# Performance work log

Hardware: AMD Instinct MI355X
Metric: run time of the kernel (lower is better)

## Reference

```python
import jax, jax.numpy as jnp
import numpy as np

D_MODEL = 1024
D_K = 1024
D_V = 1024
N_HEAD = 16
EPS = 1e-5
BS, N_TOK = 2, 2048


def setup_inputs() -> dict:
    key = jax.random.key(0)
    ks = jax.random.split(key, 12)
    s = 0.02
    q = jax.random.normal(ks[0], (BS, N_TOK, D_MODEL), jnp.float32)
    k = jax.random.normal(ks[1], (BS, N_TOK, D_MODEL), jnp.float32)
    v = jax.random.normal(ks[2], (BS, N_TOK, D_MODEL), jnp.float32)
    return {
        "q": q, "k": k, "v": v,
        "gamma": jnp.ones((D_MODEL,), jnp.float32),
        "beta": jnp.zeros((D_MODEL,), jnp.float32),
        "Wq": jax.random.normal(ks[3], (D_MODEL, D_K), jnp.float32) * s,
        "bq": jnp.zeros((D_K,), jnp.float32),
        "Wk": jax.random.normal(ks[4], (D_MODEL, D_K), jnp.float32) * s,
        "bk": jnp.zeros((D_K,), jnp.float32),
        "Wv": jax.random.normal(ks[5], (D_MODEL, D_V), jnp.float32) * s,
        "bv": jnp.zeros((D_V,), jnp.float32),
        "Wo": jax.random.normal(ks[6], (D_V, D_MODEL), jnp.float32) * s,
        "bo": jnp.zeros((D_MODEL,), jnp.float32),
    }


def reference(q, k, v, gamma, beta, Wq, bq, Wk, bk, Wv, bv, Wo, bo):
    # NOTE: original module ignores k, v args; self-attention over q.
    bs, n_tok, d_m = q.shape
    d_h = D_K // N_HEAD
    temper = float(np.sqrt(d_h))

    # LayerNorm1d over d_model
    mu = jnp.mean(q, axis=-1, keepdims=True)
    var = jnp.var(q, axis=-1, keepdims=True)
    h = (q - mu) / jnp.sqrt(var + EPS) * gamma + beta

    # projections; head split = chunk along feature dim -> [bs, H, T, d_h]
    qh = (h @ Wq + bq).reshape(bs, n_tok, N_HEAD, d_h).transpose(0, 2, 1, 3)
    kh = (h @ Wk + bk).reshape(bs, n_tok, N_HEAD, d_h).transpose(0, 2, 1, 3)
    vh = jax.nn.relu(h @ Wv + bv).reshape(bs, n_tok, N_HEAD, d_h).transpose(0, 2, 1, 3)

    scores = jnp.einsum('bhqd,bhkd->bhqk', qh, kh) / temper
    # dropout before softmax in train mode; identity in eval (deterministic ref)
    attn = jax.nn.softmax(scores, axis=-1)
    o = jnp.einsum('bhqk,bhkd->bhqd', attn, vh)  # [bs, H, T, d_h]

    # faithful to torch: view(bs, n_tok, -1) with NO head transpose (head-major merge)
    merged = o.reshape(bs, n_tok, N_HEAD * d_h)
    out = merged @ Wo + bo + q  # proj + residual
    return out
```

## Files before the change

kernel.cpp:

```cpp
#include <hip/hip_runtime.h>

typedef __bf16 bf16;
typedef __bf16 bf16x8 __attribute__((ext_vector_type(8)));
typedef __bf16 bf16x4 __attribute__((ext_vector_type(4)));
typedef float  f32x4  __attribute__((ext_vector_type(4)));
typedef float  f32x16 __attribute__((ext_vector_type(16)));
typedef unsigned int u32;
typedef u32 u32x4 __attribute__((ext_vector_type(4)));

#define AS1U(p) ((const __attribute__((address_space(1))) unsigned int*)(p))
#define AS3U(p) ((__attribute__((address_space(3))) unsigned int*)(p))

static __device__ __forceinline__ u32 pack2(float a, float b) {
    unsigned short ua = __builtin_bit_cast(unsigned short, (bf16)a);
    unsigned short ub = __builtin_bit_cast(unsigned short, (bf16)b);
    return (u32)ua | ((u32)ub << 16);
}

__global__ void transpose_cast4_kernel(const float* __restrict__ W0, const float* __restrict__ W1,
                                       const float* __restrict__ W2, const float* __restrict__ W3,
                                       bf16* __restrict__ D0, bf16* __restrict__ D1,
                                       bf16* __restrict__ D2, bf16* __restrict__ D3) {
    __shared__ float tile[32][33];
    const float* W; bf16* D;
    switch (blockIdx.z) {
        case 0: W = W0; D = D0; break;
        case 1: W = W1; D = D1; break;
        case 2: W = W2; D = D2; break;
        default: W = W3; D = D3; break;
    }
    const int bj = blockIdx.x, bi = blockIdx.y;
    const int tx = threadIdx.x, ty = threadIdx.y;
#pragma unroll
    for (int i = 0; i < 4; i++) {
        tile[ty + i * 8][tx] = W[(size_t)(bi * 32 + ty + i * 8) * 1024 + bj * 32 + tx];
    }
    __syncthreads();
#pragma unroll
    for (int i = 0; i < 4; i++) {
        D[(size_t)(bj * 32 + ty + i * 8) * 1024 + bi * 32 + tx] =
            (bf16)tile[tx][ty + i * 8];
    }
}

__global__ void layernorm_kernel(const float* __restrict__ x,
                                 const float* __restrict__ gamma,
                                 const float* __restrict__ beta,
                                 bf16* __restrict__ h) {
    const int row = blockIdx.x;
    const float* xr = x + (size_t)row * 1024;
    const int t = threadIdx.x;
    float4 v = ((const float4*)xr)[t];
    float s  = v.x + v.y + v.z + v.w;
    float s2 = v.x * v.x + v.y * v.y + v.z * v.z + v.w * v.w;
#pragma unroll
    for (int m = 1; m < 64; m <<= 1) {
        s  += __shfl_xor(s, m, 64);
        s2 += __shfl_xor(s2, m, 64);
    }
    __shared__ float ssum[4], ssum2[4];
    const int wid = t >> 6, lane = t & 63;
    if (lane == 0) { ssum[wid] = s; ssum2[wid] = s2; }
    __syncthreads();
    s  = ssum[0] + ssum[1] + ssum[2] + ssum[3];
    s2 = ssum2[0] + ssum2[1] + ssum2[2] + ssum2[3];
    const float mu  = s * (1.f / 1024.f);
    const float var = s2 * (1.f / 1024.f) - mu * mu;
    const float rs  = rsqrtf(var + 1e-5f);
    float4 g = ((const float4*)gamma)[t];
    float4 b = ((const float4*)beta)[t];
    bf16x4 o;
    o[0] = (bf16)((v.x - mu) * rs * g.x + b.x);
    o[1] = (bf16)((v.y - mu) * rs * g.y + b.y);
    o[2] = (bf16)((v.z - mu) * rs * g.z + b.z);
    o[3] = (bf16)((v.w - mu) * rs * g.w + b.w);
    ((bf16x4*)(h + (size_t)row * 1024))[t] = o;
}

template <int EPI>
__global__ void gemm_kernel(const bf16* __restrict__ A, const bf16* __restrict__ BT,
                            int N, int K,
                            bf16* __restrict__ Cb,
                            const float* __restrict__ b0, const float* __restrict__ b1,
                            const float* __restrict__ b2, bf16* __restrict__ Vt,
                            float* __restrict__ Cf, const float* __restrict__ bo,
                            const float* __restrict__ resid) {
    __shared__ bf16 Asm[128][32];
    __shared__ bf16 Bsm[128][32];
    const int tid = threadIdx.x;
    const int lane = tid & 63, wave = tid >> 6;
    const int wr = wave >> 1, wc = wave & 1;
    const int tileN = blockIdx.x * 128, tileM = blockIdx.y * 128;
    const int row16 = lane & 15, g = lane >> 4;

    f32x4 acc[4][4] = {};

    for (int kt = 0; kt < K; kt += 32) {
#pragma unroll
        for (int i = 0; i < 2; i++) {
            int c = tid + i * 256;
            int r = c >> 2, cb = (c & 3) * 16;
            const char* g_ = (const char*)(A + (size_t)(tileM + r) * K + kt) + cb;
            char* l_ = (char*)&Asm[0][0] + c * 16;
            __builtin_amdgcn_global_load_lds(AS1U(g_), AS3U(l_), 16, 0, 0);
        }
#pragma unroll
        for (int i = 0; i < 2; i++) {
            int c = tid + i * 256;
            int r = c >> 2, cb = (c & 3) * 16;
            const char* g_ = (const char*)(BT + (size_t)(tileN + r) * K + kt) + cb;
            char* l_ = (char*)&Bsm[0][0] + c * 16;
            __builtin_amdgcn_global_load_lds(AS1U(g_), AS3U(l_), 16, 0, 0);
        }
        __syncthreads();
        bf16x8 af[4], bfr[4];
#pragma unroll
        for (int m = 0; m < 4; m++)
            af[m] = *(const bf16x8*)&Asm[wr * 64 + m * 16 + row16][g * 8];
#pragma unroll
        for (int n = 0; n < 4; n++)
            bfr[n] = *(const bf16x8*)&Bsm[wc * 64 + n * 16 + row16][g * 8];
#pragma unroll
        for (int m = 0; m < 4; m++)
#pragma unroll
            for (int n = 0; n < 4; n++)
                acc[m][n] = __builtin_amdgcn_mfma_f32_16x16x32_bf16(af[m], bfr[n],
                                                                   acc[m][n], 0, 0, 0);
        __syncthreads();
    }
#pragma unroll
    for (int m = 0; m < 4; m++) {
        const int row = tileM + wr * 64 + m * 16 + g * 4;
#pragma unroll
        for (int n = 0; n < 4; n++) {
            const int col = tileN + wc * 64 + n * 16 + row16;
            if (EPI == 0 && col >= 2048) {
                const int d = col - 2048;
                const float bias = b2[d];
                bf16x4 pk;
#pragma unroll
                for (int j = 0; j < 4; j++) {
                    float v = acc[m][n][j] + bias;
                    pk[j] = (bf16)fmaxf(v, 0.f);
                }
                const int bb = row >> 11, tt = row & 2047;
                const int hh = d >> 6, dd = d & 63;
                *(bf16x4*)&Vt[(((size_t)bb * 16 + hh) * 64 + dd) * 2048 + tt] = pk;
            } else {
#pragma unroll
                for (int j = 0; j < 4; j++) {
                    float v = acc[m][n][j];
                    const int r = row + j;
                    if (EPI == 0) {
                        if (col < 1024) {
                            v = (v + b0[col]) * 0.18033688011112042f;
                        } else {
                            v += b1[col - 1024];
                        }
                        Cb[(size_t)r * N + col] = (bf16)v;
                    } else {
                        v += bo[col] + resid[(size_t)r * N + col];
                        Cf[(size_t)r * N + col] = v;
                    }
                }
            }
        }
    }
}

__global__ __launch_bounds__(512, 4)
void attn_kernel(const bf16* __restrict__ qkv, const bf16* __restrict__ Vt,
                 bf16* __restrict__ Obuf) {
    const int bid = blockIdx.x;
    const int swz = (bid & 7) * 64 + (bid >> 3);
    const int bh = swz >> 4, qt = swz & 15;
    const int b = bh >> 4, h = bh & 15;
    const int qbase = qt * 128;
    const int tid = threadIdx.x;
    const int lane = tid & 63, wv = tid >> 6;
    const int half = wv >> 2, qw = wv & 3;
    const int c = lane & 31, p = lane >> 5;

    __shared__ bf16 Kl[2][2][64][64];
    __shared__ bf16 Vl[2][2][64][64];

    const bf16* qrow = qkv + (size_t)(b * 2048 + qbase + qw * 32 + c) * 3072 + h * 64;
    bf16x8 qf[4];
#pragma unroll
    for (int ch = 0; ch < 4; ch++)
        qf[ch] = *(const bf16x8*)(qrow + ch * 16 + p * 8);

    const char* kgbase = (const char*)(qkv + (size_t)b * 2048 * 3072 + 1024 + h * 64)
                         + (size_t)(half * 1024) * 6144;
    const char* vgbase = (const char*)(Vt + (size_t)bh * 64 * 2048) + half * 2048;
    const int ht = tid & 255;
    const char* kgp[2]; const char* vgp[2]; int ldo[2];
#pragma unroll
    for (int i = 0; i < 2; i++) {
        const int cc = ht + i * 256;
        const int srow = cc >> 3;
        const int scol = ((cc & 7) * 16) ^ ((srow & 7) << 4);
        kgp[i] = kgbase + (size_t)srow * 6144 + scol;
        vgp[i] = vgbase + (size_t)srow * 4096 + scol;
        ldo[i] = cc * 16;
    }
    char* kldb = (char*)&Kl[half][0][0][0];
    char* vldb = (char*)&Vl[half][0][0][0];

    auto stage = [&](int t, int slot) {
        const size_t ko = (size_t)t * (64 * 6144);
        const size_t vo = (size_t)t * 128;
        const int sb = slot * 8192;
#pragma unroll
        for (int i = 0; i < 2; i++) {
            __builtin_amdgcn_global_load_lds(AS1U(kgp[i] + ko), AS3U(kldb + sb + ldo[i]), 16, 0, 0);
            __builtin_amdgcn_global_load_lds(AS1U(vgp[i] + vo), AS3U(vldb + sb + ldo[i]), 16, 0, 0);
        }
    };

    f32x16 accO[2] = {};
    float l_r = 0.f;

    auto compute = [&](int slot) {
        const char* Kb = (const char*)&Kl[half][slot][0][0];
        const char* Vb = (const char*)&Vl[half][slot][0][0];
#pragma unroll
        for (int cc = 0; cc < 2; cc++) {
            f32x16 accT = {};
            const int tok = cc * 32 + c;
#pragma unroll
            for (int ch = 0; ch < 4; ch++) {
                const bf16x8 kf = *(const bf16x8*)(Kb + tok * 128 +
                                                   ((ch * 32 + p * 16) ^ ((tok & 7) << 4)));
                accT = __builtin_amdgcn_mfma_f32_32x32x16_bf16(kf, qf[ch], accT, 0, 0, 0);
            }
            float pv[16];
#pragma unroll
            for (int r = 0; r < 16; r++) pv[r] = exp2f(accT[r]);
            float s01 = (pv[0] + pv[1]) + (pv[2] + pv[3]);
            float s23 = (pv[4] + pv[5]) + (pv[6] + pv[7]);
            float s45 = (pv[8] + pv[9]) + (pv[10] + pv[11]);
            float s67 = (pv[12] + pv[13]) + (pv[14] + pv[15]);
            l_r += (s01 + s23) + (s45 + s67);
            u32 k01 = pack2(pv[0], pv[1]),  k23 = pack2(pv[2], pv[3]);
            u32 k45 = pack2(pv[4], pv[5]),  k67 = pack2(pv[6], pv[7]);
            u32 k89 = pack2(pv[8], pv[9]),  kab = pack2(pv[10], pv[11]);
            u32 kcd = pack2(pv[12], pv[13]), kef = pack2(pv[14], pv[15]);
            asm("v_permlane32_swap_b32 %0, %1" : "+v"(k45), "+v"(k01));
            asm("v_permlane32_swap_b32 %0, %1" : "+v"(k67), "+v"(k23));
            asm("v_permlane32_swap_b32 %0, %1" : "+v"(kcd), "+v"(k89));
            asm("v_permlane32_swap_b32 %0, %1" : "+v"(kef), "+v"(kab));
            u32x4 w0w = {k01, k23, k45, k67};
            u32x4 w1w = {k89, kab, kcd, kef};
            const bf16x8 pf0 = __builtin_bit_cast(bf16x8, w0w);
            const bf16x8 pf1 = __builtin_bit_cast(bf16x8, w1w);
#pragma unroll
            for (int dc = 0; dc < 2; dc++) {
                const int rd = dc * 32 + c;
                const int sw = (rd & 7) << 4;
                const bf16x8 vf0 = *(const bf16x8*)(Vb + rd * 128 + ((cc * 64 + p * 16) ^ sw));
                const bf16x8 vf1 = *(const bf16x8*)(Vb + rd * 128 + ((cc * 64 + 32 + p * 16) ^ sw));
                accO[dc] = __builtin_amdgcn_mfma_f32_32x32x16_bf16(pf0, vf0, accO[dc], 0, 0, 0);
                accO[dc] = __builtin_amdgcn_mfma_f32_32x32x16_bf16(pf1, vf1, accO[dc], 0, 0, 0);
            }
        }
    };

#define KV_SYNC() do { \
        asm volatile("s_waitcnt vmcnt(0)" ::: "memory"); \
        __builtin_amdgcn_s_barrier(); \
        asm volatile("" ::: "memory"); \
    } while (0)

    stage(0, 0);
#pragma unroll 1
    for (int t = 0; t < 14; t += 2) {
        KV_SYNC(); stage(t + 1, 1); compute(0);
        KV_SYNC(); stage(t + 2, 0); compute(1);
    }
    KV_SYNC(); stage(15, 1); compute(0);
    KV_SYNC(); compute(1);
#undef KV_SYNC

    __syncthreads();
    float* ex = (float*)&Kl[0][0][0][0];
    const int xb = (qw * 64 + lane) * 33;
    if (half) {
#pragma unroll
        for (int dc = 0; dc < 2; dc++)
#pragma unroll
            for (int r = 0; r < 16; r++) ex[xb + dc * 16 + r] = accO[dc][r];
        ex[xb + 32] = l_r;
    }
    __syncthreads();
    if (!half) {
#pragma unroll
        for (int dc = 0; dc < 2; dc++)
#pragma unroll
            for (int r = 0; r < 16; r++) accO[dc][r] += ex[xb + dc * 16 + r];
        l_r += ex[xb + 32];
        l_r += __shfl_xor(l_r, 32);
        const float linv = 1.f / l_r;
        float li[16];
#pragma unroll
        for (int r = 0; r < 16; r++)
            li[r] = __shfl(linv, (r & 3) + 8 * (r >> 2) + 4 * p);
        bf16* ob = Obuf + ((size_t)bh * 2048 + qbase + qw * 32) * 64;
#pragma unroll
        for (int dc = 0; dc < 2; dc++)
#pragma unroll
            for (int r = 0; r < 16; r++) {
                const int row = (r & 3) + 8 * (r >> 2) + 4 * p;
                ob[(size_t)row * 64 + dc * 32 + c] = (bf16)(accO[dc][r] * li[r]);
            }
    }
}

extern "C" void kernel_launch(void* const* d_in, const int* in_sizes, int n_in,
                              void* d_out, int out_size, void* d_ws, size_t ws_size,
                              hipStream_t stream) {
    const float* q     = (const float*)d_in[0];
    const float* gamma = (const float*)d_in[3];
    const float* beta  = (const float*)d_in[4];
    const float* Wq    = (const float*)d_in[5];
    const float* bq    = (const float*)d_in[6];
    const float* Wk    = (const float*)d_in[7];
    const float* bk    = (const float*)d_in[8];
    const float* Wv    = (const float*)d_in[9];
    const float* bv    = (const float*)d_in[10];
    const float* Wo    = (const float*)d_in[11];
    const float* bo    = (const float*)d_in[12];
    float* out = (float*)d_out;

    char* ws = (char*)d_ws;
    bf16* h     = (bf16*)(ws);
    bf16* WcatT = (bf16*)(ws + (8u << 20));
    bf16* WoT   = (bf16*)(ws + (14u << 20));
    bf16* qkv   = (bf16*)(ws + (16u << 20));
    bf16* Obuf  = (bf16*)(ws + (40u << 20));
    bf16* Vtb   = (bf16*)(ws + (48u << 20));

    transpose_cast4_kernel<<<dim3(32, 32, 4), dim3(32, 8), 0, stream>>>(
        Wq, Wk, Wv, Wo,
        WcatT, WcatT + (size_t)1024 * 1024, WcatT + (size_t)2048 * 1024, WoT);

    layernorm_kernel<<<4096, 256, 0, stream>>>(q, gamma, beta, h);

    gemm_kernel<0><<<dim3(24, 32), 256, 0, stream>>>(h, WcatT, 3072, 1024,
                                                     qkv, bq, bk, bv, Vtb,
                                                     nullptr, nullptr, nullptr);

    attn_kernel<<<512, 512, 0, stream>>>(qkv, Vtb, Obuf);

    gemm_kernel<1><<<dim3(8, 32), 256, 0, stream>>>(Obuf, WoT, 1024, 1024,
                                                    nullptr, nullptr, nullptr, nullptr, nullptr,
                                                    out, bo, q);
}
```

Measured before the change: 143.5 us.

## Stage QKV GEMM epilogue through swizzled LDS for coalesced stores; remap block order

The QKV projection epilogue now writes biased, scaled and activated results into a per-wave XOR-swizzled LDS tile, then reads them back as 16-byte rows and stores them coalesced to the Q/K buffer or the transposed V buffer. This replaces the old scattered 2-byte and 8-byte strided global stores. The block index is also remapped so that consecutive workgroups are spread in strides of eight across the tile grid, which changes L2 reuse and XCD placement. The cost is an extra 32 KB of shared memory per block, which can lower occupancy, plus an LDS round trip in the epilogue.

New measurement: 131.2 us. 1.09x faster.

```diff
diff --git a/kernel.cpp b/kernel.cpp
--- a/kernel.cpp
+++ b/kernel.cpp
@@ -90,7 +90,11 @@
     const int tid = threadIdx.x;
     const int lane = tid & 63, wave = tid >> 6;
     const int wr = wave >> 1, wc = wave & 1;
-    const int tileN = blockIdx.x * 128, tileM = blockIdx.y * 128;
+    const int nwg = gridDim.x * gridDim.y;
+    const int bid0 = blockIdx.y * gridDim.x + blockIdx.x;
+    const int bid = (bid0 & 7) * (nwg >> 3) + (bid0 >> 3);
+    const int tileN = (bid % gridDim.x) * 128;
+    const int tileM = (bid / gridDim.x) * 128;
     const int row16 = lane & 15, g = lane >> 4;
 
     f32x4 acc[4][4] = {};
@@ -128,40 +132,79 @@
                                                                    acc[m][n], 0, 0, 0);
         __syncthreads();
     }
-#pragma unroll
-    for (int m = 0; m < 4; m++) {
-        const int row = tileM + wr * 64 + m * 16 + g * 4;
-#pragma unroll
-        for (int n = 0; n < 4; n++) {
-            const int col = tileN + wc * 64 + n * 16 + row16;
-            if (EPI == 0 && col >= 2048) {
-                const int d = col - 2048;
-                const float bias = b2[d];
-                bf16x4 pk;
+
+    if constexpr (EPI == 0) {
+        __shared__ bf16 Ep[4][64][64];
+        char* ep = (char*)&Ep[wave][0][0];
+        const bool isV = (tileN >= 2048);
+        if (!isV) {
+#pragma unroll
+            for (int n = 0; n < 4; n++) {
+                const int cl = n * 16 + row16;
+                const int gc = tileN + wc * 64 + cl;
+                const float bias = gc < 1024 ? b0[gc] : b1[gc - 1024];
+                const float scl = gc < 1024 ? 0.18033688011112042f : 1.f;
+#pragma unroll
+                for (int m = 0; m < 4; m++)
+#pragma unroll
+                    for (int j = 0; j < 4; j++) {
+                        const int rl = m * 16 + g * 4 + j;
+                        const float v = (acc[m][n][j] + bias) * scl;
+                        *(bf16*)(ep + rl * 128 + ((cl * 2) ^ ((rl & 7) << 4))) = (bf16)v;
+                    }
+            }
+        } else {
+#pragma unroll
+            for (int n = 0; n < 4; n++) {
+                const int dl = n * 16 + row16;
+                const float bias = b2[(tileN - 2048) + wc * 64 + dl];
+#pragma unroll
+                for (int m = 0; m < 4; m++)
+#pragma unroll
+                    for (int j = 0; j < 4; j++) {
+                        const int tl = m * 16 + g * 4 + j;
+                        const float v = fmaxf(acc[m][n][j] + bias, 0.f);
+                        *(bf16*)(ep + dl * 128 + ((tl * 2) ^ ((dl & 7) << 4))) = (bf16)v;
+                    }
+            }
+        }
+        asm volatile("s_waitcnt lgkmcnt(0)" ::: "memory");
+        __builtin_amdgcn_sched_barrier(0);
+        if (!isV) {
+#pragma unroll
+            for (int it = 0; it < 8; it++) {
+                const int rl = (lane >> 3) + it * 8;
+                const bf16x8 vrow = *(const bf16x8*)(ep + rl * 128 +
+                                                     (((lane & 7) * 16) ^ ((rl & 7) << 4)));
+                const int gr = tileM + wr * 64 + rl;
+                const int gc = tileN + wc * 64 + (lane & 7) * 8;
+                *(bf16x8*)&Cb[(size_t)gr * N + gc] = vrow;
+            }
+        } else {
+            const int bb = tileM >> 11;
+            const int tbase = (tileM & 2047) + wr * 64 + (lane & 7) * 8;
+#pragma unroll
+            for (int it = 0; it < 8; it++) {
+                const int dl = (lane >> 3) + it * 8;
+                const bf16x8 vrow = *(const bf16x8*)(ep + dl * 128 +
+                                                     (((lane & 7) * 16) ^ ((dl & 7) << 4)));
+                const int gd = (tileN - 2048) + wc * 64 + dl;
+                const int hh = gd >> 6, dd = gd & 63;
+                *(bf16x8*)&Vt[(((size_t)bb * 16 + hh) * 64 + dd) * 2048 + tbase] = vrow;
+            }
+        }
+    } else {
+#pragma unroll
+        for (int m = 0; m < 4; m++) {
+            const int row = tileM + wr * 64 + m * 16 + g * 4;
+#pragma unroll
+            for (int n = 0; n < 4; n++) {
+                const int col = tileN + wc * 64 + n * 16 + row16;
 #pragma unroll
                 for (int j = 0; j < 4; j++) {
-                    float v = acc[m][n][j] + bias;
-                    pk[j] = (bf16)fmaxf(v, 0.f);
-                }
-                const int bb = row >> 11, tt = row & 2047;
-                const int hh = d >> 6, dd = d & 63;
-                *(bf16x4*)&Vt[(((size_t)bb * 16 + hh) * 64 + dd) * 2048 + tt] = pk;
-            } else {
-#pragma unroll
-                for (int j = 0; j < 4; j++) {
-                    float v = acc[m][n][j];
                     const int r = row + j;
-                    if (EPI == 0) {
-                        if (col < 1024) {
-                            v = (v + b0[col]) * 0.18033688011112042f;
-                        } else {
-                            v += b1[col - 1024];
-                        }
-                        Cb[(size_t)r * N + col] = (bf16)v;
-                    } else {
-                        v += bo[col] + resid[(size_t)r * N + col];
-                        Cf[(size_t)r * N + col] = v;
-                    }
+                    Cf[(size_t)r * N + col] = acc[m][n][j] + bo[col] +
+                                              resid[(size_t)r * N + col];
                 }
             }
         }
```
